# Kernel tuning notes

Hardware: AMD Instinct MI355X
Metric: run time of the kernel (lower is better)

The kernel has to match this reference:

```python
import jax, jax.numpy as jnp
import numpy as np
from jax.scipy.special import logsumexp

EPS = 0.1
NUM_ITERS = 50
TOPO_MULT = 1.0


def _dist_cosine(x):
    # x: [N, D] -> pairwise cosine distance [N, N], clamped to >= 0
    norms = jnp.sqrt(jnp.clip(jnp.sum(x * x, axis=1, keepdims=True), 1e-8, None))
    xn = x / norms
    return jnp.clip(1.0 - xn @ xn.T, 0.0, None)


def _sinkhorn_log_domain(a, b, C):
    # a, b: [N, N] row-stochastic; C: [N, N]. Duals computed with no grad (detached).
    log_a = jnp.log(jnp.clip(a, 1e-8, None))
    log_b = jnp.log(jnp.clip(b, 1e-8, None))
    la = jax.lax.stop_gradient(log_a)
    lb = jax.lax.stop_gradient(log_b)
    lC = jax.lax.stop_gradient(-C / EPS)[None]  # [1, N, N]

    def body(i, fg):
        f, g = fg
        g = EPS * lb - EPS * logsumexp(f[:, :, None] + lC, axis=1)
        f = EPS * la - EPS * logsumexp(lC + g[:, None, :], axis=2)
        return (f, g)

    f0 = jnp.zeros_like(a)
    f, g = jax.lax.fori_loop(0, NUM_ITERS, body, (f0, f0))
    cost = jnp.sum(a * f, axis=1) + jnp.sum(b * g, axis=1)  # [N]
    return jnp.mean(cost)


def reference(x_original, x_reconstructed, z_latent, log_sigma_lat, log_var_recon, log_var_topo):
    recon_loss = jnp.mean((x_reconstructed - x_original) ** 2)

    D_orig = _dist_cosine(x_original)   # [N, N]
    D_latent = _dist_cosine(z_latent)   # [N, N]

    sigma_orig = jnp.median(D_orig)
    sigma_orig = jnp.where(sigma_orig == 0, jnp.asarray(1e-6, D_orig.dtype), sigma_orig)
    sigma_lat = jax.nn.softplus(log_sigma_lat) + 1e-6  # [1]

    S_orig = jnp.exp(-D_orig ** 2 / (2.0 * sigma_orig ** 2))
    S_lat = jnp.exp(-D_latent ** 2 / (2.0 * sigma_lat ** 2))

    N = S_orig.shape[0]
    mask = 1.0 - jnp.eye(N, dtype=S_orig.dtype)
    S_orig = S_orig * mask
    S_lat = S_lat * mask

    P_orig = S_orig / jnp.clip(jnp.sum(S_orig, axis=1, keepdims=True), 1e-8, None)
    P_lat = S_lat / jnp.clip(jnp.sum(S_lat, axis=1, keepdims=True), 1e-8, None)

    C = D_orig
    ot_orig_lat = _sinkhorn_log_domain(P_orig, P_lat, C)
    ot_lat_lat = _sinkhorn_log_domain(P_lat, P_lat, C)
    ot_orig_orig = _sinkhorn_log_domain(P_orig, P_orig, C)

    topo_loss = jnp.clip(ot_orig_lat - 0.5 * ot_lat_lat - 0.5 * ot_orig_orig, 0.0, None)
    topo_loss = topo_loss * TOPO_MULT

    prec_r = jnp.exp(-log_var_recon)  # [1]
    prec_t = jnp.exp(-log_var_topo)   # [1]
    total_loss = (0.5 * prec_r * recon_loss + 0.5 * log_var_recon
                  + 0.5 * prec_t * topo_loss + 0.5 * log_var_topo)  # [1]
    return (total_loss, recon_loss, topo_loss)


def setup_inputs() -> dict:
    key = jax.random.key(0)
    k1, k2, k3 = jax.random.split(key, 3)
    N, D, DL = 256, 4096, 256
    return {
        "x_original": jax.random.normal(k1, (N, D), dtype=jnp.float32),
        "x_reconstructed": jax.random.normal(k2, (N, D), dtype=jnp.float32),
        "z_latent": jax.random.normal(k3, (N, DL), dtype=jnp.float32),
        "log_sigma_lat": jnp.zeros((1,), dtype=jnp.float32),
        "log_var_recon": jnp.zeros((1,), dtype=jnp.float32),
        "log_var_topo": jnp.zeros((1,), dtype=jnp.float32),
    }
```

## Files before the change

### kernel.cpp

```cpp
#include <hip/hip_runtime.h>
#include <hip/hip_fp16.h>

#define EPS 0.1f
#define SINK_ITERS 50
#define KSCALE_LN 9.0109133472f
#define USTRIDE 272

typedef _Float16 f16;
typedef _Float16 f16x4 __attribute__((ext_vector_type(4)));
typedef _Float16 f16x8 __attribute__((ext_vector_type(8)));
typedef float f32x4 __attribute__((ext_vector_type(4)));

#define PIN_U4(v) asm volatile("" : "+v"(v.x), "+v"(v.y), "+v"(v.z), "+v"(v.w))

__device__ __forceinline__ float wave_red_sum(float v) {
    #pragma unroll
    for (int o = 32; o; o >>= 1) v += __shfl_xor(v, o, 64);
    return v;
}

__global__ __launch_bounds__(256) void k_pre(const float4* __restrict__ xo,
                                             const float4* __restrict__ xr,
                                             const float4* __restrict__ z,
                                             f16x4* __restrict__ xh,
                                             f16x4* __restrict__ zh,
                                             float* __restrict__ acc) {
    __shared__ float red[4];
    int b = blockIdx.x, t = threadIdx.x;
    if (b < 512) {
        int tid = b * 256 + t;
        float s = 0.f;
        for (int i = tid; i < 262144; i += 512 * 256) {
            float4 a = xo[i], r = xr[i];
            float d0 = r.x - a.x, d1 = r.y - a.y, d2 = r.z - a.z, d3 = r.w - a.w;
            s = fmaf(d0, d0, s); s = fmaf(d1, d1, s);
            s = fmaf(d2, d2, s); s = fmaf(d3, d3, s);
        }
        s = wave_red_sum(s);
        if ((t & 63) == 0) red[t >> 6] = s;
        __syncthreads();
        if (t == 0) atomicAdd(acc + 3, red[0] + red[1] + red[2] + red[3]);
    } else {
        int row = b - 512;
        const float4* src; f16x4* dst; int c4;
        if (row < 256) { src = xo + (size_t)row * 1024; dst = xh + (size_t)row * 1024; c4 = 1024; }
        else { src = z + (size_t)(row - 256) * 64; dst = zh + (size_t)(row - 256) * 64; c4 = 64; }
        float s = 0.f;
        for (int i = t; i < c4; i += 256) {
            float4 v = src[i];
            s = fmaf(v.x, v.x, s); s = fmaf(v.y, v.y, s);
            s = fmaf(v.z, v.z, s); s = fmaf(v.w, v.w, s);
        }
        s = wave_red_sum(s);
        if ((t & 63) == 0) red[t >> 6] = s;
        __syncthreads();
        float tot = red[0] + red[1] + red[2] + red[3];
        float rn = 1.f / sqrtf(fmaxf(tot, 1e-8f));
        for (int i = t; i < c4; i += 256) {
            float4 v = src[i];
            f16x4 h;
            h[0] = (f16)(v.x * rn); h[1] = (f16)(v.y * rn);
            h[2] = (f16)(v.z * rn); h[3] = (f16)(v.w * rn);
            dst[i] = h;
        }
    }
}

__global__ __launch_bounds__(256) void k_gemm_f16(const uint4* __restrict__ xh,
                                                  const uint4* __restrict__ zh,
                                                  float* __restrict__ part,
                                                  float* __restrict__ part2) {
    __shared__ __align__(16) f16 Ai[64 * 40], Bj[64 * 40];
    int zb = blockIdx.z;
    const uint4* X; int lda8, k0, nchunk; float* out;
    if (zb < 16) { X = xh; lda8 = 512; k0 = zb * 256; nchunk = 8; out = part + (size_t)zb * 65536; }
    else { X = zh; lda8 = 32; k0 = (zb - 16) * 64; nchunk = 2; out = part2 + (size_t)(zb - 16) * 65536; }
    int i0 = blockIdx.x * 64, j0 = blockIdx.y * 64;
    int t = threadIdx.x, lane = t & 63, wv = t >> 6;
    int m16 = lane & 15, quad = lane >> 4;
    int r = t >> 2, ko = (t & 3) * 8;
    f32x4 acc[4] = {};
    for (int ch = 0; ch < nchunk; ch++) {
        int kb8 = (k0 + ch * 32) >> 3;
        uint4 va = X[(size_t)(i0 + r) * lda8 + kb8 + (t & 3)];
        uint4 vb = X[(size_t)(j0 + r) * lda8 + kb8 + (t & 3)];
        __syncthreads();
        *(uint4*)&Ai[r * 40 + ko] = va;
        *(uint4*)&Bj[r * 40 + ko] = vb;
        __syncthreads();
        f16x8 a = *(const f16x8*)&Ai[(wv * 16 + m16) * 40 + quad * 8];
        #pragma unroll
        for (int st = 0; st < 4; st++) {
            f16x8 bfr = *(const f16x8*)&Bj[(st * 16 + m16) * 40 + quad * 8];
            acc[st] = __builtin_amdgcn_mfma_f32_16x16x32_f16(a, bfr, acc[st], 0, 0, 0);
        }
    }
    #pragma unroll
    for (int st = 0; st < 4; st++)
        #pragma unroll
        for (int reg = 0; reg < 4; reg++)
            out[(i0 + wv * 16 + quad * 4 + reg) * 256 + j0 + st * 16 + m16] = acc[st][reg];
}

__global__ __launch_bounds__(256) void k_reduce_do(const float* __restrict__ part,
                                                   float* __restrict__ Do) {
    int e = blockIdx.x * 256 + threadIdx.x;
    float s = 0.f;
    for (int sl = 0; sl < 16; sl++) s += part[(size_t)sl * 65536 + e];
    Do[e] = fmaxf(1.f - s, 0.f);
}

__device__ __forceinline__ int med_bin(float v) {
    int b = (int)(v * 4096.f);
    if (v < (float)b * (1.f / 4096.f)) b--;
    else if (v >= (float)(b + 1) * (1.f / 4096.f)) b++;
    if (b < 0) b = 0;
    if (b > 8191) b = 8191;
    return b;
}

__global__ __launch_bounds__(1024) void k_median(const float* __restrict__ D,
                                                 float* __restrict__ out_sigma) {
    __shared__ int hist[8192];
    __shared__ int redc[16];
    __shared__ int sh_bin[2];
    __shared__ int sh_tot;
    int t = threadIdx.x;
    unsigned r[64];
    #pragma unroll
    for (int i = 0; i < 64; i++) r[i] = __float_as_uint(D[t + i * 1024]);
    #pragma unroll
    for (int j = 0; j < 8; j++) hist[t + j * 1024] = 0;
    __syncthreads();
    #pragma unroll
    for (int i = 0; i < 64; i++)
        atomicAdd(&hist[med_bin(__uint_as_float(r[i]))], 1);
    __syncthreads();
    int s8 = 0;
    #pragma unroll
    for (int j = 0; j < 8; j++) s8 += hist[t * 8 + j];
    int inc = s8;
    #pragma unroll
    for (int o = 1; o < 64; o <<= 1) {
        int vv = __shfl_up(inc, o, 64);
        if ((t & 63) >= o) inc += vv;
    }
    if ((t & 63) == 63) redc[t >> 6] = inc;
    __syncthreads();
    int woff = 0;
    for (int wv = 0; wv < (t >> 6); wv++) woff += redc[wv];
    int excl = woff + inc - s8;
    for (int sel = 0; sel < 2; sel++) {
        int k = 32767 + sel;
        if (excl <= k && k < excl + s8) {
            int cum = excl, bfound = 8191;
            bool found = false;
            for (int j = 0; j < 8; j++) {
                int hc = hist[t * 8 + j];
                if (!found) {
                    if (cum + hc > k) { bfound = t * 8 + j; found = true; }
                    else cum += hc;
                }
            }
            sh_bin[sel] = bfound;
        }
    }
    __syncthreads();
    unsigned res[2];
    for (int sel = 0; sel < 2; sel++) {
        int k = 32767 + sel;
        int b = sh_bin[sel];
        unsigned lo = __float_as_uint((float)b * (1.f / 4096.f));
        unsigned hi = __float_as_uint((float)(b + 1) * (1.f / 4096.f));
        while (hi - lo > 1u) {
            unsigned mid = (lo + hi) >> 1;
            int c = 0;
            #pragma unroll
            for (int i = 0; i < 64; i++) c += (r[i] < mid) ? 1 : 0;
            #pragma unroll
            for (int o = 32; o; o >>= 1) c += __shfl_xor(c, o, 64);
            if ((t & 63) == 0) redc[t >> 6] = c;
            __syncthreads();
            if (t == 0) {
                int tot = 0;
                for (int wv = 0; wv < 16; wv++) tot += redc[wv];
                sh_tot = tot;
            }
            __syncthreads();
            if (sh_tot <= k) lo = mid; else hi = mid;
        }
        res[sel] = lo;
    }
    if (t == 0)
        out_sigma[0] = 0.5f * (__uint_as_float(res[0]) + __uint_as_float(res[1]));
}

__global__ __launch_bounds__(256) void k_prep(const float* __restrict__ Do,
                                              const float* __restrict__ part2,
                                              const float* __restrict__ wsacc,
                                              const float* __restrict__ lsl,
                                              float* __restrict__ Po, float* __restrict__ Pl,
                                              float* __restrict__ ELo, float* __restrict__ ELl,
                                              f16* __restrict__ Kh) {
    __shared__ float red[8];
    int i = blockIdx.x, j = threadIdx.x;
    int e = i * 256 + j;
    float sig_o = wsacc[4];
    if (sig_o == 0.f) sig_o = 1e-6f;
    float x = lsl[0];
    float sp = (x > 20.f) ? x : log1pf(__expf(x));
    float sig_l = sp + 1e-6f;
    float i2o = 1.f / (2.f * sig_o * sig_o);
    float i2l = 1.f / (2.f * sig_l * sig_l);
    float d_o = Do[e];
    float sD = part2[e] + part2[65536 + e] + part2[131072 + e] + part2[196608 + e];
    float d_l = fmaxf(1.f - sD, 0.f);
    float so = (i == j) ? 0.f : __expf(-d_o * d_o * i2o);
    float sl = (i == j) ? 0.f : __expf(-d_l * d_l * i2l);
    float wso = wave_red_sum(so);
    float wsl = wave_red_sum(sl);
    if ((j & 63) == 0) { red[j >> 6] = wso; red[4 + (j >> 6)] = wsl; }
    __syncthreads();
    float sum_o = red[0] + red[1] + red[2] + red[3];
    float sum_l = red[4] + red[5] + red[6] + red[7];
    float po = so / fmaxf(sum_o, 1e-8f);
    float pl = sl / fmaxf(sum_l, 1e-8f);
    Po[e] = po;
    Pl[e] = pl;
    ELo[e] = EPS * __logf(fmaxf(po, 1e-8f));
    ELl[e] = EPS * __logf(fmaxf(pl, 1e-8f));
    float kv = __expf(-d_o * (1.f / EPS) + KSCALE_LN);
    Kh[(((i >> 3) * 256 + j) << 3) + (i & 7)] = (f16)kv;
}

__global__ __launch_bounds__(512, 2) void k_sinkhorn(const float* __restrict__ Po,
                                                     const float* __restrict__ Pl,
                                                     const float* __restrict__ ELo,
                                                     const float* __restrict__ ELl,
                                                     const uint4* __restrict__ Kq,
                                                     float* __restrict__ wsacc) {
    __shared__ __align__(16) f16 U[2][4 * USTRIDE];
    __shared__ float CW[8][4];
    int t = threadIdx.x;
    int lane = t & 63, wv = t >> 6;
    int m16 = lane & 15, quad = lane >> 4;
    int w = blockIdx.x;
    int s = w >> 6;
    int ibase = (w & 63) * 4;

    uint4 bf0[8], bf1[8];
    int cA = 32 * wv + m16, cB = cA + 16;
    #pragma unroll
    for (int kc = 0; kc < 8; kc++) {
        bf0[kc] = Kq[(kc * 4 + quad) * 256 + cA];
        bf1[kc] = Kq[(kc * 4 + quad) * 256 + cB];
    }
    #pragma unroll
    for (int kc = 0; kc < 8; kc++) { PIN_U4(bf0[kc]); PIN_U4(bf1[kc]); }

    const float* ELa_b = (s == 1 ? ELl : ELo);
    const float* ELb_b = (s == 2 ? ELo : ELl);
    float ela[2][4] = {}, elb[2][4] = {};
    if (quad == 0) {
        #pragma unroll
        for (int reg = 0; reg < 4; reg++) {
            int i = ibase + reg;
            ela[0][reg] = ELa_b[i * 256 + cA] + EPS * KSCALE_LN;
            ela[1][reg] = ELa_b[i * 256 + cB] + EPS * KSCALE_LN;
            elb[0][reg] = ELb_b[i * 256 + cA] + EPS * KSCALE_LN;
            elb[1][reg] = ELb_b[i * 256 + cB] + EPS * KSCALE_LN;
        }
    }

    if (t < 136)
        *(uint4*)&U[0][t * 8] =
            make_uint4(0x3C003C00u, 0x3C003C00u, 0x3C003C00u, 0x3C003C00u);
    __syncthreads();

    float df[2][4] = {}, dg[2][4] = {};
    for (int it = 0; it < 2 * SINK_ITERS; it++) {
        const f16* ub = &U[it & 1][0];
        f16* un = &U[(it + 1) & 1][0];
        f32x4 acc0 = {0.f, 0.f, 0.f, 0.f}, acc1 = {0.f, 0.f, 0.f, 0.f};
        #pragma unroll
        for (int kc = 0; kc < 8; kc++) {
            f16x8 a = *(const f16x8*)&ub[(m16 & 3) * USTRIDE + kc * 32 + quad * 8];
            acc0 = __builtin_amdgcn_mfma_f32_16x16x32_f16(a, __builtin_bit_cast(f16x8, bf0[kc]),
                                                          acc0, 0, 0, 0);
            acc1 = __builtin_amdgcn_mfma_f32_16x16x32_f16(a, __builtin_bit_cast(f16x8, bf1[kc]),
                                                          acc1, 0, 0, 0);
        }
        bool fstep = (it & 1);
        if (quad == 0) {
            #pragma unroll
            for (int reg = 0; reg < 4; reg++) {
                float z0 = acc0[reg], z1 = acc1[reg];
                float e0 = fstep ? ela[0][reg] : elb[0][reg];
                float e1 = fstep ? ela[1][reg] : elb[1][reg];
                float d0 = e0 - EPS * __logf(z0);
                float d1 = e1 - EPS * __logf(z1);
                if (fstep) { df[0][reg] = d0; df[1][reg] = d1; }
                else       { dg[0][reg] = d0; dg[1][reg] = d1; }
                un[reg * USTRIDE + cA] = (f16)__expf(d0);
                un[reg * USTRIDE + cB] = (f16)__expf(d1);
            }
        }
        __syncthreads();
    }

    const float* PaB = (s == 1 ? Pl : Po);
    const float* PbB = (s == 2 ? Po : Pl);
    float cs[4] = {};
    if (quad == 0) {
        #pragma unroll
        for (int reg = 0; reg < 4; reg++) {
            int i = ibase + reg;
            cs[reg] = PaB[i * 256 + cA] * df[0][reg] + PbB[i * 256 + cA] * dg[0][reg] +
                      PaB[i * 256 + cB] * df[1][reg] + PbB[i * 256 + cB] * dg[1][reg];
        }
    }
    #pragma unroll
    for (int o = 1; o < 16; o <<= 1) {
        #pragma unroll
        for (int reg = 0; reg < 4; reg++) cs[reg] += __shfl_xor(cs[reg], o, 64);
    }
    if (lane == 0) {
        #pragma unroll
        for (int reg = 0; reg < 4; reg++) CW[wv][reg] = cs[reg];
    }
    __syncthreads();
    if (t == 0) {
        float v = 0.f;
        for (int w2 = 0; w2 < 8; w2++)
            v += CW[w2][0] + CW[w2][1] + CW[w2][2] + CW[w2][3];
        atomicAdd(&wsacc[s], v);
    }
}

__global__ void k_final(const float* __restrict__ wsacc, const float* __restrict__ lvr_p,
                        const float* __restrict__ lvt_p, float* __restrict__ out) {
    float recon = wsacc[3] * (1.f / (256.f * 4096.f));
    float ot0 = wsacc[0] * (1.f / 256.f);
    float ot1 = wsacc[1] * (1.f / 256.f);
    float ot2 = wsacc[2] * (1.f / 256.f);
    float topo = ot0 - 0.5f * ot1 - 0.5f * ot2;
    topo = topo > 0.f ? topo : 0.f;
    float lvr = lvr_p[0], lvt = lvt_p[0];
    out[0] = 0.5f * __expf(-lvr) * recon + 0.5f * lvr +
             0.5f * __expf(-lvt) * topo + 0.5f * lvt;
    out[1] = recon;
    out[2] = topo;
}

extern "C" void kernel_launch(void* const* d_in, const int* in_sizes, int n_in,
                              void* d_out, int out_size, void* d_ws, size_t ws_size,
                              hipStream_t stream) {
    const float* xo = (const float*)d_in[0];
    const float* xr = (const float*)d_in[1];
    const float* z  = (const float*)d_in[2];
    const float* lsl = (const float*)d_in[3];
    const float* lvr = (const float*)d_in[4];
    const float* lvt = (const float*)d_in[5];
    float* out = (float*)d_out;
    float* ws = (float*)d_ws;

    float* acc = ws;
    float* xh  = ws + 64;
    float* zh  = xh + 524288;
    float* Do  = zh + 32768;
    float* Po  = Do + 65536;
    float* Pl  = Po + 65536;
    float* ELo = Pl + 65536;
    float* ELl = ELo + 65536;
    float* Kh  = ELl + 65536;
    float* part = Kh + 32768;
    float* part2 = Po;

    hipMemsetAsync(acc, 0, 64, stream);
    k_pre<<<1024, 256, 0, stream>>>((const float4*)xo, (const float4*)xr, (const float4*)z,
                                    (f16x4*)xh, (f16x4*)zh, acc);
    k_gemm_f16<<<dim3(4, 4, 20), 256, 0, stream>>>((const uint4*)xh, (const uint4*)zh,
                                                   part, part2);
    k_reduce_do<<<256, 256, 0, stream>>>(part, Do);
    k_median<<<1, 1024, 0, stream>>>(Do, acc + 4);
    k_prep<<<256, 256, 0, stream>>>(Do, part2, acc, lsl, Po, Pl, ELo, ELl, (f16*)Kh);
    k_sinkhorn<<<192, 512, 0, stream>>>(Po, Pl, ELo, ELl, (const uint4*)Kh, acc);
    k_final<<<1, 1, 0, stream>>>(acc, lvr, lvt, out);
}
```

Before: 223.1 us.

## Fuse whole pipeline into one cooperative persistent kernel with grid syncs

New measurement: 396.5 us. 77.7% more time.

```diff
diff --git a/kernel.cpp b/kernel.cpp
--- a/kernel.cpp
+++ b/kernel.cpp
@@ -1,10 +1,12 @@
 #include <hip/hip_runtime.h>
+#include <hip/hip_cooperative_groups.h>
 #include <hip/hip_fp16.h>
+
+namespace cg = cooperative_groups;
 
 #define EPS 0.1f
 #define SINK_ITERS 50
 #define KSCALE_LN 9.0109133472f
-#define USTRIDE 272
 
 typedef _Float16 f16;
 typedef _Float16 f16x4 __attribute__((ext_vector_type(4)));
@@ -18,97 +20,19 @@
     for (int o = 32; o; o >>= 1) v += __shfl_xor(v, o, 64);
     return v;
 }
-
-__global__ __launch_bounds__(256) void k_pre(const float4* __restrict__ xo,
-                                             const float4* __restrict__ xr,
-                                             const float4* __restrict__ z,
-                                             f16x4* __restrict__ xh,
-                                             f16x4* __restrict__ zh,
-                                             float* __restrict__ acc) {
-    __shared__ float red[4];
-    int b = blockIdx.x, t = threadIdx.x;
-    if (b < 512) {
-        int tid = b * 256 + t;
-        float s = 0.f;
-        for (int i = tid; i < 262144; i += 512 * 256) {
-            float4 a = xo[i], r = xr[i];
-            float d0 = r.x - a.x, d1 = r.y - a.y, d2 = r.z - a.z, d3 = r.w - a.w;
-            s = fmaf(d0, d0, s); s = fmaf(d1, d1, s);
-            s = fmaf(d2, d2, s); s = fmaf(d3, d3, s);
-        }
-        s = wave_red_sum(s);
-        if ((t & 63) == 0) red[t >> 6] = s;
-        __syncthreads();
-        if (t == 0) atomicAdd(acc + 3, red[0] + red[1] + red[2] + red[3]);
-    } else {
-        int row = b - 512;
-        const float4* src; f16x4* dst; int c4;
-        if (row < 256) { src = xo + (size_t)row * 1024; dst = xh + (size_t)row * 1024; c4 = 1024; }
-        else { src = z + (size_t)(row - 256) * 64; dst = zh + (size_t)(row - 256) * 64; c4 = 64; }
-        float s = 0.f;
-        for (int i = t; i < c4; i += 256) {
-            float4 v = src[i];
-            s = fmaf(v.x, v.x, s); s = fmaf(v.y, v.y, s);
-            s = fmaf(v.z, v.z, s); s = fmaf(v.w, v.w, s);
-        }
-        s = wave_red_sum(s);
-        if ((t & 63) == 0) red[t >> 6] = s;
-        __syncthreads();
-        float tot = red[0] + red[1] + red[2] + red[3];
-        float rn = 1.f / sqrtf(fmaxf(tot, 1e-8f));
-        for (int i = t; i < c4; i += 256) {
-            float4 v = src[i];
-            f16x4 h;
-            h[0] = (f16)(v.x * rn); h[1] = (f16)(v.y * rn);
-            h[2] = (f16)(v.z * rn); h[3] = (f16)(v.w * rn);
-            dst[i] = h;
-        }
-    }
-}
-
-__global__ __launch_bounds__(256) void k_gemm_f16(const uint4* __restrict__ xh,
-                                                  const uint4* __restrict__ zh,
-                                                  float* __restrict__ part,
-                                                  float* __restrict__ part2) {
-    __shared__ __align__(16) f16 Ai[64 * 40], Bj[64 * 40];
-    int zb = blockIdx.z;
-    const uint4* X; int lda8, k0, nchunk; float* out;
-    if (zb < 16) { X = xh; lda8 = 512; k0 = zb * 256; nchunk = 8; out = part + (size_t)zb * 65536; }
-    else { X = zh; lda8 = 32; k0 = (zb - 16) * 64; nchunk = 2; out = part2 + (size_t)(zb - 16) * 65536; }
-    int i0 = blockIdx.x * 64, j0 = blockIdx.y * 64;
-    int t = threadIdx.x, lane = t & 63, wv = t >> 6;
-    int m16 = lane & 15, quad = lane >> 4;
-    int r = t >> 2, ko = (t & 3) * 8;
-    f32x4 acc[4] = {};
-    for (int ch = 0; ch < nchunk; ch++) {
-        int kb8 = (k0 + ch * 32) >> 3;
-        uint4 va = X[(size_t)(i0 + r) * lda8 + kb8 + (t & 3)];
-        uint4 vb = X[(size_t)(j0 + r) * lda8 + kb8 + (t & 3)];
-        __syncthreads();
-        *(uint4*)&Ai[r * 40 + ko] = va;
-        *(uint4*)&Bj[r * 40 + ko] = vb;
-        __syncthreads();
-        f16x8 a = *(const f16x8*)&Ai[(wv * 16 + m16) * 40 + quad * 8];
-        #pragma unroll
-        for (int st = 0; st < 4; st++) {
-            f16x8 bfr = *(const f16x8*)&Bj[(st * 16 + m16) * 40 + quad * 8];
-            acc[st] = __builtin_amdgcn_mfma_f32_16x16x32_f16(a, bfr, acc[st], 0, 0, 0);
-        }
-    }
+__device__ __forceinline__ int wave_red_sum_i(int v) {
     #pragma unroll
-    for (int st = 0; st < 4; st++)
-        #pragma unroll
-        for (int reg = 0; reg < 4; reg++)
-            out[(i0 + wv * 16 + quad * 4 + reg) * 256 + j0 + st * 16 + m16] = acc[st][reg];
-}
-
-__global__ __launch_bounds__(256) void k_reduce_do(const float* __restrict__ part,
-                                                   float* __restrict__ Do) {
-    int e = blockIdx.x * 256 + threadIdx.x;
-    float s = 0.f;
-    for (int sl = 0; sl < 16; sl++) s += part[(size_t)sl * 65536 + e];
-    Do[e] = fmaxf(1.f - s, 0.f);
-}
+    for (int o = 32; o; o >>= 1) v += __shfl_xor(v, o, 64);
+    return v;
+}
+
+union __align__(16) SM {
+    struct { f16 Ai[64 * 40]; f16 Bj[64 * 40]; } g;
+    struct { f16 U[4 * 272]; float ZP[256][4]; float CW[4][3]; } s;
+    struct { float a[8]; float b[8]; } r;
+    struct { int redc[8]; int bin[2]; int tot; } m;
+    float red[8];
+};
 
 __device__ __forceinline__ int med_bin(float v) {
     int b = (int)(v * 4096.f);
@@ -119,271 +43,367 @@
     return b;
 }
 
-__global__ __launch_bounds__(1024) void k_median(const float* __restrict__ D,
-                                                 float* __restrict__ out_sigma) {
-    __shared__ int hist[8192];
-    __shared__ int redc[16];
-    __shared__ int sh_bin[2];
-    __shared__ int sh_tot;
-    int t = threadIdx.x;
-    unsigned r[64];
+__device__ __forceinline__ void gemm_unit(const uint4* __restrict__ X, int lda8,
+                                          int i0, int j0, int kb8_0,
+                                          float* __restrict__ out, SM& sm, int t) {
+    int lane = t & 63, wv = t >> 6, m16 = lane & 15, quad = lane >> 4;
+    int rr = (t & 255) >> 2, kk = t & 3;
+    int rbase = (t < 256) ? i0 : j0;
+    f16* stg = (t < 256) ? sm.g.Ai : sm.g.Bj;
+    f32x4 a0 = {0.f, 0.f, 0.f, 0.f}, a1 = {0.f, 0.f, 0.f, 0.f};
+    for (int ch = 0; ch < 8; ch++) {
+        uint4 v = X[(size_t)(rbase + rr) * lda8 + kb8_0 + ch * 4 + kk];
+        __syncthreads();
+        *(uint4*)&stg[rr * 40 + kk * 8] = v;
+        __syncthreads();
+        f16x8 a  = *(const f16x8*)&sm.g.Ai[((wv & 3) * 16 + m16) * 40 + quad * 8];
+        f16x8 b0 = *(const f16x8*)&sm.g.Bj[((wv >> 2) * 32 + m16) * 40 + quad * 8];
+        f16x8 b1 = *(const f16x8*)&sm.g.Bj[((wv >> 2) * 32 + 16 + m16) * 40 + quad * 8];
+        a0 = __builtin_amdgcn_mfma_f32_16x16x32_f16(a, b0, a0, 0, 0, 0);
+        a1 = __builtin_amdgcn_mfma_f32_16x16x32_f16(a, b1, a1, 0, 0, 0);
+    }
+    int orow = i0 + (wv & 3) * 16 + quad * 4;
+    int ocol = j0 + (wv >> 2) * 32 + m16;
     #pragma unroll
-    for (int i = 0; i < 64; i++) r[i] = __float_as_uint(D[t + i * 1024]);
+    for (int reg = 0; reg < 4; reg++) {
+        out[(orow + reg) * 256 + ocol] = a0[reg];
+        out[(orow + reg) * 256 + ocol + 16] = a1[reg];
+    }
+}
+
+__device__ __forceinline__ void prep_a_row(int row, int t, SM& sm,
+                                           const float* __restrict__ part2,
+                                           const float* __restrict__ Do,
+                                           const float* __restrict__ lsl,
+                                           float* __restrict__ Pl, float* __restrict__ ELl,
+                                           f16* __restrict__ Kh) {
+    float x = lsl[0];
+    float sp = (x > 20.f) ? x : log1pf(__expf(x));
+    float sgl = sp + 1e-6f;
+    float i2l = 1.f / (2.f * sgl * sgl);
+    float slv = 0.f, dov = 0.f;
+    if (t < 256) {
+        int e = row * 256 + t;
+        float dl = fmaxf(1.f - part2[e], 0.f);
+        slv = (row == t) ? 0.f : __expf(-dl * dl * i2l);
+        dov = Do[e];
+    }
+    float ws = wave_red_sum(slv);
+    if ((t & 63) == 0) sm.red[t >> 6] = ws;
+    __syncthreads();
+    float tot = sm.red[0] + sm.red[1] + sm.red[2] + sm.red[3];
+    if (t < 256) {
+        int e = row * 256 + t;
+        float pl = slv / fmaxf(tot, 1e-8f);
+        Pl[e] = pl;
+        ELl[e] = EPS * __logf(fmaxf(pl, 1e-8f));
+        float kv = __expf(-dov * (1.f / EPS) + KSCALE_LN);
+        Kh[(((row >> 3) * 256 + t) << 3) + (row & 7)] = (f16)kv;
+    }
+    __syncthreads();
+}
+
+__device__ __forceinline__ void prep_b_row(int row, int t, SM& sm,
+                                           const float* __restrict__ Do,
+                                           const float* __restrict__ acc,
+                                           float* __restrict__ Po, float* __restrict__ ELo) {
+    float sg = acc[4];
+    if (sg == 0.f) sg = 1e-6f;
+    float i2o = 1.f / (2.f * sg * sg);
+    float sov = 0.f;
+    if (t < 256) {
+        float dov = Do[row * 256 + t];
+        sov = (row == t) ? 0.f : __expf(-dov * dov * i2o);
+    }
+    float ws = wave_red_sum(sov);
+    if ((t & 63) == 0) sm.red[t >> 6] = ws;
+    __syncthreads();
+    float tot = sm.red[0] + sm.red[1] + sm.red[2] + sm.red[3];
+    if (t < 256) {
+        int e = row * 256 + t;
+        float po = sov / fmaxf(tot, 1e-8f);
+        Po[e] = po;
+        ELo[e] = EPS * __logf(fmaxf(po, 1e-8f));
+    }
+    __syncthreads();
+}
+
+__device__ void median_phase(const float* __restrict__ Do, const int* __restrict__ hist,
+                             float* __restrict__ acc, SM& sm, int t) {
+    int lane = t & 63, wv = t >> 6;
+    unsigned r[128];
     #pragma unroll
-    for (int j = 0; j < 8; j++) hist[t + j * 1024] = 0;
-    __syncthreads();
-    #pragma unroll
-    for (int i = 0; i < 64; i++)
-        atomicAdd(&hist[med_bin(__uint_as_float(r[i]))], 1);
-    __syncthreads();
-    int s8 = 0;
-    #pragma unroll
-    for (int j = 0; j < 8; j++) s8 += hist[t * 8 + j];
-    int inc = s8;
+    for (int i = 0; i < 128; i++) r[i] = __float_as_uint(Do[t + i * 512]);
+    int base = t * 16;
+    int s16 = 0;
+    for (int j = 0; j < 16; j++) s16 += hist[base + j];
+    int inc = s16;
     #pragma unroll
     for (int o = 1; o < 64; o <<= 1) {
         int vv = __shfl_up(inc, o, 64);
-        if ((t & 63) >= o) inc += vv;
-    }
-    if ((t & 63) == 63) redc[t >> 6] = inc;
+        if (lane >= o) inc += vv;
+    }
+    if (lane == 63) sm.m.redc[wv] = inc;
     __syncthreads();
     int woff = 0;
-    for (int wv = 0; wv < (t >> 6); wv++) woff += redc[wv];
-    int excl = woff + inc - s8;
+    for (int i = 0; i < wv; i++) woff += sm.m.redc[i];
+    int excl = woff + inc - s16;
     for (int sel = 0; sel < 2; sel++) {
         int k = 32767 + sel;
-        if (excl <= k && k < excl + s8) {
+        if (excl <= k && k < excl + s16) {
             int cum = excl, bfound = 8191;
             bool found = false;
-            for (int j = 0; j < 8; j++) {
-                int hc = hist[t * 8 + j];
+            for (int j = 0; j < 16; j++) {
+                int hc = hist[base + j];
                 if (!found) {
-                    if (cum + hc > k) { bfound = t * 8 + j; found = true; }
+                    if (cum + hc > k) { bfound = base + j; found = true; }
                     else cum += hc;
                 }
             }
-            sh_bin[sel] = bfound;
+            sm.m.bin[sel] = bfound;
         }
     }
     __syncthreads();
     unsigned res[2];
     for (int sel = 0; sel < 2; sel++) {
         int k = 32767 + sel;
-        int b = sh_bin[sel];
-        unsigned lo = __float_as_uint((float)b * (1.f / 4096.f));
-        unsigned hi = __float_as_uint((float)(b + 1) * (1.f / 4096.f));
+        int bb = sm.m.bin[sel];
+        unsigned lo = __float_as_uint((float)bb * (1.f / 4096.f));
+        unsigned hi = __float_as_uint((float)(bb + 1) * (1.f / 4096.f));
         while (hi - lo > 1u) {
             unsigned mid = (lo + hi) >> 1;
             int c = 0;
             #pragma unroll
-            for (int i = 0; i < 64; i++) c += (r[i] < mid) ? 1 : 0;
-            #pragma unroll
-            for (int o = 32; o; o >>= 1) c += __shfl_xor(c, o, 64);
-            if ((t & 63) == 0) redc[t >> 6] = c;
+            for (int i = 0; i < 128; i++) c += (r[i] < mid) ? 1 : 0;
+            c = wave_red_sum_i(c);
+            if (lane == 0) sm.m.redc[wv] = c;
             __syncthreads();
             if (t == 0) {
                 int tot = 0;
-                for (int wv = 0; wv < 16; wv++) tot += redc[wv];
-                sh_tot = tot;
+                for (int i = 0; i < 8; i++) tot += sm.m.redc[i];
+                sm.m.tot = tot;
             }
             __syncthreads();
-            if (sh_tot <= k) lo = mid; else hi = mid;
+            if (sm.m.tot <= k) lo = mid; else hi = mid;
         }
         res[sel] = lo;
     }
     if (t == 0)
-        out_sigma[0] = 0.5f * (__uint_as_float(res[0]) + __uint_as_float(res[1]));
-}
-
-__global__ __launch_bounds__(256) void k_prep(const float* __restrict__ Do,
-                                              const float* __restrict__ part2,
-                                              const float* __restrict__ wsacc,
-                                              const float* __restrict__ lsl,
-                                              float* __restrict__ Po, float* __restrict__ Pl,
-                                              float* __restrict__ ELo, float* __restrict__ ELl,
-                                              f16* __restrict__ Kh) {
-    __shared__ float red[8];
-    int i = blockIdx.x, j = threadIdx.x;
-    int e = i * 256 + j;
-    float sig_o = wsacc[4];
-    if (sig_o == 0.f) sig_o = 1e-6f;
-    float x = lsl[0];
-    float sp = (x > 20.f) ? x : log1pf(__expf(x));
-    float sig_l = sp + 1e-6f;
-    float i2o = 1.f / (2.f * sig_o * sig_o);
-    float i2l = 1.f / (2.f * sig_l * sig_l);
-    float d_o = Do[e];
-    float sD = part2[e] + part2[65536 + e] + part2[131072 + e] + part2[196608 + e];
-    float d_l = fmaxf(1.f - sD, 0.f);
-    float so = (i == j) ? 0.f : __expf(-d_o * d_o * i2o);
-    float sl = (i == j) ? 0.f : __expf(-d_l * d_l * i2l);
-    float wso = wave_red_sum(so);
-    float wsl = wave_red_sum(sl);
-    if ((j & 63) == 0) { red[j >> 6] = wso; red[4 + (j >> 6)] = wsl; }
-    __syncthreads();
-    float sum_o = red[0] + red[1] + red[2] + red[3];
-    float sum_l = red[4] + red[5] + red[6] + red[7];
-    float po = so / fmaxf(sum_o, 1e-8f);
-    float pl = sl / fmaxf(sum_l, 1e-8f);
-    Po[e] = po;
-    Pl[e] = pl;
-    ELo[e] = EPS * __logf(fmaxf(po, 1e-8f));
-    ELl[e] = EPS * __logf(fmaxf(pl, 1e-8f));
-    float kv = __expf(-d_o * (1.f / EPS) + KSCALE_LN);
-    Kh[(((i >> 3) * 256 + j) << 3) + (i & 7)] = (f16)kv;
-}
-
-__global__ __launch_bounds__(512, 2) void k_sinkhorn(const float* __restrict__ Po,
-                                                     const float* __restrict__ Pl,
-                                                     const float* __restrict__ ELo,
-                                                     const float* __restrict__ ELl,
-                                                     const uint4* __restrict__ Kq,
-                                                     float* __restrict__ wsacc) {
-    __shared__ __align__(16) f16 U[2][4 * USTRIDE];
-    __shared__ float CW[8][4];
-    int t = threadIdx.x;
-    int lane = t & 63, wv = t >> 6;
-    int m16 = lane & 15, quad = lane >> 4;
-    int w = blockIdx.x;
-    int s = w >> 6;
-    int ibase = (w & 63) * 4;
-
-    uint4 bf0[8], bf1[8];
-    int cA = 32 * wv + m16, cB = cA + 16;
-    #pragma unroll
-    for (int kc = 0; kc < 8; kc++) {
-        bf0[kc] = Kq[(kc * 4 + quad) * 256 + cA];
-        bf1[kc] = Kq[(kc * 4 + quad) * 256 + cB];
-    }
-    #pragma unroll
-    for (int kc = 0; kc < 8; kc++) { PIN_U4(bf0[kc]); PIN_U4(bf1[kc]); }
-
-    const float* ELa_b = (s == 1 ? ELl : ELo);
-    const float* ELb_b = (s == 2 ? ELo : ELl);
-    float ela[2][4] = {}, elb[2][4] = {};
-    if (quad == 0) {
+        acc[4] = 0.5f * (__uint_as_float(res[0]) + __uint_as_float(res[1]));
+}
+
+__global__ __launch_bounds__(512, 2) void k_fused(const float4* __restrict__ xo4,
+                                                  const float4* __restrict__ xr4,
+                                                  const float4* __restrict__ z4,
+                                                  const float* __restrict__ lsl,
+                                                  const float* __restrict__ lvr,
+                                                  const float* __restrict__ lvt,
+                                                  float* __restrict__ out,
+                                                  float* __restrict__ ws) {
+    cg::grid_group grid = cg::this_grid();
+    __shared__ SM sm;
+    const int b = blockIdx.x, t = threadIdx.x;
+    const int lane = t & 63, wv = t >> 6, m16 = lane & 15, quad = lane >> 4;
+
+    float* acc = ws;
+    int* hist = (int*)(ws + 64);
+    f16* xh = (f16*)(ws + 64 + 8192);
+    f16* zh = xh + 1048576;
+    float* Do = (float*)(zh + 65536);
+    float* Po = Do + 65536;
+    float* Pl = Po + 65536;
+    float* ELo = Pl + 65536;
+    float* ELl = ELo + 65536;
+    f16* Kh = (f16*)(ELl + 65536);
+    float* part = (float*)(Kh + 65536);
+    float* part2 = part + 16 * 65536;
+
+    {
+        if (t < 64) {
+            float4 vz = z4[(size_t)b * 64 + t];
+            float sz = vz.x * vz.x + vz.y * vz.y + vz.z * vz.z + vz.w * vz.w;
+            sz = wave_red_sum(sz);
+            float rnz = 1.f / sqrtf(fmaxf(sz, 1e-8f));
+            f16x4 h;
+            h[0] = (f16)(vz.x * rnz); h[1] = (f16)(vz.y * rnz);
+            h[2] = (f16)(vz.z * rnz); h[3] = (f16)(vz.w * rnz);
+            *(f16x4*)&zh[(size_t)b * 256 + t * 4] = h;
+        }
+        size_t ro = (size_t)b * 1024;
+        float4 v0 = xo4[ro + t], v1 = xo4[ro + t + 512];
+        float4 r0 = xr4[ro + t], r1 = xr4[ro + t + 512];
+        float sq = v0.x * v0.x + v0.y * v0.y + v0.z * v0.z + v0.w * v0.w
+                 + v1.x * v1.x + v1.y * v1.y + v1.z * v1.z + v1.w * v1.w;
+        float d0 = r0.x - v0.x, d1 = r0.y - v0.y, d2 = r0.z - v0.z, d3 = r0.w - v0.w;
+        float e0 = r1.x - v1.x, e1 = r1.y - v1.y, e2 = r1.z - v1.z, e3 = r1.w - v1.w;
+        float rs = d0 * d0 + d1 * d1 + d2 * d2 + d3 * d3
+                 + e0 * e0 + e1 * e1 + e2 * e2 + e3 * e3;
+        float wq = wave_red_sum(sq), wr = wave_red_sum(rs);
+        if (lane == 0) { sm.r.a[wv] = wq; sm.r.b[wv] = wr; }
+        __syncthreads();
+        float tq = 0.f, tr = 0.f;
         #pragma unroll
-        for (int reg = 0; reg < 4; reg++) {
-            int i = ibase + reg;
-            ela[0][reg] = ELa_b[i * 256 + cA] + EPS * KSCALE_LN;
-            ela[1][reg] = ELa_b[i * 256 + cB] + EPS * KSCALE_LN;
-            elb[0][reg] = ELb_b[i * 256 + cA] + EPS * KSCALE_LN;
-            elb[1][reg] = ELb_b[i * 256 + cB] + EPS * KSCALE_LN;
-        }
-    }
-
-    if (t < 136)
-        *(uint4*)&U[0][t * 8] =
-            make_uint4(0x3C003C00u, 0x3C003C00u, 0x3C003C00u, 0x3C003C00u);
-    __syncthreads();
-
-    float df[2][4] = {}, dg[2][4] = {};
-    for (int it = 0; it < 2 * SINK_ITERS; it++) {
-        const f16* ub = &U[it & 1][0];
-        f16* un = &U[(it + 1) & 1][0];
-        f32x4 acc0 = {0.f, 0.f, 0.f, 0.f}, acc1 = {0.f, 0.f, 0.f, 0.f};
+        for (int i = 0; i < 8; i++) { tq += sm.r.a[i]; tr += sm.r.b[i]; }
+        if (t == 0) atomicAdd(acc + 3, tr);
+        float rn = 1.f / sqrtf(fmaxf(tq, 1e-8f));
+        f16x4 h0, h1;
+        h0[0] = (f16)(v0.x * rn); h0[1] = (f16)(v0.y * rn);
+        h0[2] = (f16)(v0.z * rn); h0[3] = (f16)(v0.w * rn);
+        h1[0] = (f16)(v1.x * rn); h1[1] = (f16)(v1.y * rn);
+        h1[2] = (f16)(v1.z * rn); h1[3] = (f16)(v1.w * rn);
+        *(f16x4*)&xh[(size_t)b * 4096 + t * 4] = h0;
+        *(f16x4*)&xh[(size_t)b * 4096 + 2048 + t * 4] = h1;
+    }
+    grid.sync();
+
+    {
+        int tile = b >> 4, slab = b & 15;
+        gemm_unit((const uint4*)xh, 512, (tile >> 2) * 64, (tile & 3) * 64,
+                  slab * 32, part + (size_t)slab * 65536, sm, t);
+        if (b >= 240) {
+            int tl = b - 240;
+            gemm_unit((const uint4*)zh, 32, (tl >> 2) * 64, (tl & 3) * 64, 0, part2, sm, t);
+        }
+    }
+    grid.sync();
+
+    if (t < 256) {
+        int e = b * 256 + t;
+        float s = 0.f;
+        for (int sl = 0; sl < 16; sl++) s += part[(size_t)sl * 65536 + e];
+        float dv = fmaxf(1.f - s, 0.f);
+        Do[e] = dv;
+        atomicAdd(&hist[med_bin(dv)], 1);
+    }
+    grid.sync();
+
+    if (b == 0) {
+        median_phase(Do, hist, acc, sm, t);
+    } else {
+        prep_a_row(b - 1, t, sm, part2, Do, lsl, Pl, ELl, Kh);
+        if (b == 255) prep_a_row(255, t, sm, part2, Do, lsl, Pl, ELl, Kh);
+    }
+    grid.sync();
+
+    prep_b_row(b, t, sm, Do, acc, Po, ELo);
+    grid.sync();
+
+    {
+        const uint4* Kq = (const uint4*)Kh;
+        uint4 bf[4][8];
+        float ela[3] = {}, elb[3] = {};
+        const float* pa[3]; const float* pb[3];
+        pa[0] = pa[1] = pa[2] = Po; pb[0] = pb[1] = pb[2] = Po;
+        if (t < 256) {
+            #pragma unroll
+            for (int st = 0; st < 4; st++)
+                #pragma unroll
+                for (int kc = 0; kc < 8; kc++)
+                    bf[st][kc] = Kq[(kc * 4 + quad) * 256 + wv * 64 + st * 16 + m16];
+            #pragma unroll
+            for (int st = 0; st < 4; st++)
+                #pragma unroll
+                for (int kc = 0; kc < 8; kc++) PIN_U4(bf[st][kc]);
+            #pragma unroll
+            for (int p = 0; p < 3; p++) {
+                int rr = b * 3 + p, s = rr >> 8, ii = rr & 255;
+                const float* ea = (s == 1 ? ELl : ELo) + ii * 256;
+                const float* eb = (s == 2 ? ELo : ELl) + ii * 256;
+                ela[p] = ea[t] + EPS * KSCALE_LN;
+                elb[p] = eb[t] + EPS * KSCALE_LN;
+                pa[p] = (s == 1 ? Pl : Po) + ii * 256;
+                pb[p] = (s == 2 ? Po : Pl) + ii * 256;
+            }
+        }
+        if (t < 136)
+            *(uint4*)&sm.s.U[t * 8] =
+                make_uint4(0x3C003C00u, 0x3C003C00u, 0x3C003C00u, 0x3C003C00u);
+        __syncthreads();
+
+        float fv[3] = {}, gv[3] = {};
+        for (int it = 0; it < 2 * SINK_ITERS; it++) {
+            if (t < 256) {
+                f32x4 a0 = {0.f,0.f,0.f,0.f}, a1 = {0.f,0.f,0.f,0.f};
+                f32x4 a2 = {0.f,0.f,0.f,0.f}, a3 = {0.f,0.f,0.f,0.f};
+                #pragma unroll
+                for (int kc = 0; kc < 8; kc++) {
+                    f16x8 a = *(const f16x8*)&sm.s.U[(m16 & 3) * 272 + kc * 32 + quad * 8];
+                    a0 = __builtin_amdgcn_mfma_f32_16x16x32_f16(a, __builtin_bit_cast(f16x8, bf[0][kc]), a0, 0, 0, 0);
+                    a1 = __builtin_amdgcn_mfma_f32_16x16x32_f16(a, __builtin_bit_cast(f16x8, bf[1][kc]), a1, 0, 0, 0);
+                    a2 = __builtin_amdgcn_mfma_f32_16x16x32_f16(a, __builtin_bit_cast(f16x8, bf[2][kc]), a2, 0, 0, 0);
+                    a3 = __builtin_amdgcn_mfma_f32_16x16x32_f16(a, __builtin_bit_cast(f16x8, bf[3][kc]), a3, 0, 0, 0);
+                }
+                if (quad == 0) {
+                    *(f32x4*)&sm.s.ZP[wv * 64 + m16][0] = a0;
+                    *(f32x4*)&sm.s.ZP[wv * 64 + 16 + m16][0] = a1;
+                    *(f32x4*)&sm.s.ZP[wv * 64 + 32 + m16][0] = a2;
+                    *(f32x4*)&sm.s.ZP[wv * 64 + 48 + m16][0] = a3;
+                }
+            }
+            __syncthreads();
+            if (t < 256) {
+                f32x4 zz = *(const f32x4*)&sm.s.ZP[t][0];
+                bool fstep = (it & 1);
+                #pragma unroll
+                for (int p = 0; p < 3; p++) {
+                    float el = fstep ? ela[p] : elb[p];
+                    float d = el - EPS * __logf(zz[p]);
+                    if (fstep) fv[p] = d; else gv[p] = d;
+                    sm.s.U[p * 272 + t] = (f16)__expf(d);
+                }
+            }
+            __syncthreads();
+        }
+
+        float cs[3] = {};
+        if (t < 256) {
+            #pragma unroll
+            for (int p = 0; p < 3; p++)
+                cs[p] = pa[p][t] * fv[p] + pb[p][t] * gv[p];
+        }
         #pragma unroll
-        for (int kc = 0; kc < 8; kc++) {
-            f16x8 a = *(const f16x8*)&ub[(m16 & 3) * USTRIDE + kc * 32 + quad * 8];
-            acc0 = __builtin_amdgcn_mfma_f32_16x16x32_f16(a, __builtin_bit_cast(f16x8, bf0[kc]),
-                                                          acc0, 0, 0, 0);
-            acc1 = __builtin_amdgcn_mfma_f32_16x16x32_f16(a, __builtin_bit_cast(f16x8, bf1[kc]),
-                                                          acc1, 0, 0, 0);
-        }
-        bool fstep = (it & 1);
-        if (quad == 0) {
-            #pragma unroll
-            for (int reg = 0; reg < 4; reg++) {
-                float z0 = acc0[reg], z1 = acc1[reg];
-                float e0 = fstep ? ela[0][reg] : elb[0][reg];
-                float e1 = fstep ? ela[1][reg] : elb[1][reg];
-                float d0 = e0 - EPS * __logf(z0);
-                float d1 = e1 - EPS * __logf(z1);
-                if (fstep) { df[0][reg] = d0; df[1][reg] = d1; }
-                else       { dg[0][reg] = d0; dg[1][reg] = d1; }
-                un[reg * USTRIDE + cA] = (f16)__expf(d0);
-                un[reg * USTRIDE + cB] = (f16)__expf(d1);
-            }
+        for (int p = 0; p < 3; p++) {
+            float v = wave_red_sum(cs[p]);
+            if (lane == 0 && wv < 4) sm.s.CW[wv][p] = v;
         }
         __syncthreads();
-    }
-
-    const float* PaB = (s == 1 ? Pl : Po);
-    const float* PbB = (s == 2 ? Po : Pl);
-    float cs[4] = {};
-    if (quad == 0) {
-        #pragma unroll
-        for (int reg = 0; reg < 4; reg++) {
-            int i = ibase + reg;
-            cs[reg] = PaB[i * 256 + cA] * df[0][reg] + PbB[i * 256 + cA] * dg[0][reg] +
-                      PaB[i * 256 + cB] * df[1][reg] + PbB[i * 256 + cB] * dg[1][reg];
-        }
-    }
-    #pragma unroll
-    for (int o = 1; o < 16; o <<= 1) {
-        #pragma unroll
-        for (int reg = 0; reg < 4; reg++) cs[reg] += __shfl_xor(cs[reg], o, 64);
-    }
-    if (lane == 0) {
-        #pragma unroll
-        for (int reg = 0; reg < 4; reg++) CW[wv][reg] = cs[reg];
-    }
-    __syncthreads();
-    if (t == 0) {
-        float v = 0.f;
-        for (int w2 = 0; w2 < 8; w2++)
-            v += CW[w2][0] + CW[w2][1] + CW[w2][2] + CW[w2][3];
-        atomicAdd(&wsacc[s], v);
-    }
-}
-
-__global__ void k_final(const float* __restrict__ wsacc, const float* __restrict__ lvr_p,
-                        const float* __restrict__ lvt_p, float* __restrict__ out) {
-    float recon = wsacc[3] * (1.f / (256.f * 4096.f));
-    float ot0 = wsacc[0] * (1.f / 256.f);
-    float ot1 = wsacc[1] * (1.f / 256.f);
-    float ot2 = wsacc[2] * (1.f / 256.f);
-    float topo = ot0 - 0.5f * ot1 - 0.5f * ot2;
-    topo = topo > 0.f ? topo : 0.f;
-    float lvr = lvr_p[0], lvt = lvt_p[0];
-    out[0] = 0.5f * __expf(-lvr) * recon + 0.5f * lvr +
-             0.5f * __expf(-lvt) * topo + 0.5f * lvt;
-    out[1] = recon;
-    out[2] = topo;
+        if (t < 3) {
+            float sv = sm.s.CW[0][t] + sm.s.CW[1][t] + sm.s.CW[2][t] + sm.s.CW[3][t];
+            atomicAdd(&acc[(b * 3 + t) >> 8], sv);
+        }
+    }
+    grid.sync();
+
+    if (b == 0 && t == 0) {
+        float recon = acc[3] * (1.f / (256.f * 4096.f));
+        float ot0 = acc[0] * (1.f / 256.f);
+        float ot1 = acc[1] * (1.f / 256.f);
+        float ot2 = acc[2] * (1.f / 256.f);
+        float topo = ot0 - 0.5f * ot1 - 0.5f * ot2;
+        topo = topo > 0.f ? topo : 0.f;
+        float a = lvr[0], c = lvt[0];
+        out[0] = 0.5f * __expf(-a) * recon + 0.5f * a +
+                 0.5f * __expf(-c) * topo + 0.5f * c;
+        out[1] = recon;
+        out[2] = topo;
+    }
 }
 
 extern "C" void kernel_launch(void* const* d_in, const int* in_sizes, int n_in,
                               void* d_out, int out_size, void* d_ws, size_t ws_size,
                               hipStream_t stream) {
-    const float* xo = (const float*)d_in[0];
-    const float* xr = (const float*)d_in[1];
-    const float* z  = (const float*)d_in[2];
+    const float4* xo4 = (const float4*)d_in[0];
+    const float4* xr4 = (const float4*)d_in[1];
+    const float4* z4  = (const float4*)d_in[2];
     const float* lsl = (const float*)d_in[3];
     const float* lvr = (const float*)d_in[4];
     const float* lvt = (const float*)d_in[5];
     float* out = (float*)d_out;
     float* ws = (float*)d_ws;
 
-    float* acc = ws;
-    float* xh  = ws + 64;
-    float* zh  = xh + 524288;
-    float* Do  = zh + 32768;
-    float* Po  = Do + 65536;
-    float* Pl  = Po + 65536;
-    float* ELo = Pl + 65536;
-    float* ELl = ELo + 65536;
-    float* Kh  = ELl + 65536;
-    float* part = Kh + 32768;
-    float* part2 = Po;
-
-    hipMemsetAsync(acc, 0, 64, stream);
-    k_pre<<<1024, 256, 0, stream>>>((const float4*)xo, (const float4*)xr, (const float4*)z,
-                                    (f16x4*)xh, (f16x4*)zh, acc);
-    k_gemm_f16<<<dim3(4, 4, 20), 256, 0, stream>>>((const uint4*)xh, (const uint4*)zh,
-                                                   part, part2);
-    k_reduce_do<<<256, 256, 0, stream>>>(part, Do);
-    k_median<<<1, 1024, 0, stream>>>(Do, acc + 4);
-    k_prep<<<256, 256, 0, stream>>>(Do, part2, acc, lsl, Po, Pl, ELo, ELl, (f16*)Kh);
-    k_sinkhorn<<<192, 512, 0, stream>>>(Po, Pl, ELo, ELl, (const uint4*)Kh, acc);
-    k_final<<<1, 1, 0, stream>>>(acc, lvr, lvt, out);
-}
+    hipMemsetAsync(ws, 0, (64 + 8192) * sizeof(float), stream);
+
+    void* kargs[] = {(void*)&xo4, (void*)&xr4, (void*)&z4, (void*)&lsl,
+                     (void*)&lvr, (void*)&lvt, (void*)&out, (void*)&ws};
+    hipLaunchCooperativeKernel((void*)k_fused, dim3(256), dim3(512), kargs, 0, stream);
+}
```
